# Kernel tuning notes

Hardware: AMD Instinct MI355X
Metric: run time of the kernel (lower is better)

## Reference

```python
import jax, jax.numpy as jnp
import numpy as np

TEMP = 0.1
NEG = -1e30  # stands in for removing the diagonal via masked_select
EPS = 1e-12  # F.normalize eps


def _l2norm(x, axis):
    n = jnp.linalg.norm(x, axis=axis, keepdims=True)
    return x / jnp.maximum(n, EPS)


def setup_inputs() -> dict:
    key = jax.random.key(0)
    k = jax.random.split(key, 6)
    B, D = 8192, 128      # instance batch, embed dim
    Bp, P = 256, 256      # patch batch, patches per sample
    v1_ins = jax.random.normal(k[0], (B, D), jnp.float32)
    v2_ins = jax.random.normal(k[1], (B, D), jnp.float32)
    v1_patch = jax.random.normal(k[2], (Bp, D, P), jnp.float32)
    v2_patch = jax.random.normal(k[3], (Bp, D, P), jnp.float32)
    v1_counts = jax.random.randint(k[4], (Bp, P), 0, 50, dtype=jnp.int32)
    v2_counts = jax.random.randint(k[5], (Bp, P), 0, 50, dtype=jnp.int32)
    return {"v1_ins": v1_ins, "v2_ins": v2_ins,
            "v1_patch": v1_patch, "v2_patch": v2_patch,
            "v1_counts": v1_counts, "v2_counts": v2_counts}


def _instance_ce(v1, v2):
    B = v1.shape[0]
    embs = jnp.concatenate([_l2norm(v1, 1), _l2norm(v2, 1)], axis=0)  # [2B, D]
    logits = (embs @ embs.T) / TEMP                                    # [2B, 2B]
    N = 2 * B
    # masking the diagonal to -inf == masked_select removal; positive of row i
    # is column (i+B) mod 2B (matches labels after diagonal removal shift)
    logits = jnp.where(jnp.eye(N, dtype=bool), NEG, logits)
    labels = jnp.concatenate([jnp.arange(B) + B, jnp.arange(B)])
    logp = jax.nn.log_softmax(logits, axis=1)
    return -jnp.mean(logp[jnp.arange(N), labels])


def _patch_ce(v1, v2, c1, c2):
    Bp, D, P = v1.shape
    embs = jnp.concatenate([_l2norm(v1, 1), _l2norm(v2, 1)], axis=2)   # [Bp, D, 2P]
    logits = jnp.einsum('bdi,bdj->bij', embs, embs) / TEMP             # [Bp, 2P, 2P]
    N = 2 * P
    logits = jnp.where(jnp.eye(N, dtype=bool)[None], NEG, logits)
    labels = jnp.concatenate([jnp.arange(P) + P, jnp.arange(P)])       # [2P]
    valid = ~jnp.concatenate([c1 == 0, c2 == 0], axis=1)               # [Bp, 2P]
    logp = jax.nn.log_softmax(logits, axis=2)
    pos = logp[:, jnp.arange(N), labels]                               # [Bp, 2P]
    # ignore_index=-100 -> mean over non-ignored elements
    n_valid = jnp.sum(valid.astype(logits.dtype))
    return -jnp.sum(jnp.where(valid, pos, 0.0)) / n_valid


def reference(v1_ins, v2_ins, v1_patch, v2_patch, v1_counts, v2_counts):
    ins_ce = _instance_ce(v1_ins, v2_ins)
    patch_ce = _patch_ce(v1_patch, v2_patch, v1_counts, v2_counts)
    return ins_ce + patch_ce
```

## Files before the change

### kernel.cpp

```cpp
#include <hip/hip_runtime.h>
#include <math.h>

typedef __bf16 bf16_t;
typedef __bf16 bf16x8 __attribute__((ext_vector_type(8)));
typedef float f32x4 __attribute__((ext_vector_type(4)));
typedef float f32x2 __attribute__((ext_vector_type(2)));

#define B_INS 8192
#define N_INS 16384
#define D 128
#define BP 256
#define P 256
#define NP 512

#define C1_CONST 14.426950408889634f

#define WS_ACC 0
#define WS_POS 8
#define WS_PPOS (WS_POS + N_INS)
#define NPAIRI 8128
#define WS_CI (WS_PPOS + BP * NP)
#define WS_RI (WS_CI + NPAIRI * 256)
#define WS_CP (WS_RI + 1088 * 256)
#define WS_RP (WS_CP + BP * 6 * 256)
#define WS_END (WS_RP + 1024 * 256)
#define EMB_I_BYTE ((((WS_END) * 4 + 15) / 16) * 16)
#define EMB_P_BYTE (EMB_I_BYTE + N_INS * D * 2)


#define NB_NORMI 128
#define NB_NORMP 2048
#define NB_PREP (NB_NORMI + NB_NORMP + 1)
#define NB_INS 1088
#define NB_PATCHB 1024
#define NB_GRAM (NB_INS + NB_PATCHB)
#define NB_FIN (128 + 256)

__device__ __forceinline__ void load_lds16(const bf16_t* g, bf16_t* l) {
    __builtin_amdgcn_global_load_lds(
        (const __attribute__((address_space(1))) void*)g,
        (__attribute__((address_space(3))) void*)l, 16, 0, 0);
}

__device__ __forceinline__ void stage_panel(const bf16_t* __restrict__ src,
                                            bf16_t* dst, int w, int lane) {
    const bf16_t* g = src + w * 4096 + lane * 8;
    bf16_t* d = dst + w * 4096;
#pragma unroll
    for (int it = 0; it < 8; it++)
        load_lds16(g + it * 512, d + it * 512);
}

__device__ __forceinline__ void load_afrags(const bf16_t* __restrict__ abase,
                                            int rh, int tx, int q, bf16x8 af[4][4]) {
    const bf16_t* a = abase + ((rh * 64 + tx) << 3);
#pragma unroll
    for (int rt = 0; rt < 4; rt++)
#pragma unroll
        for (int ks = 0; ks < 4; ks++)
            af[rt][ks] = *(const bf16x8*)(a + (((ks << 2) + q) << 10) + (rt << 7));
}

__global__ __launch_bounds__(256) void prep_k(const float* __restrict__ v1i,
                                              const float* __restrict__ v2i,
                                              const float* __restrict__ v1p,
                                              const float* __restrict__ v2p,
                                              bf16_t* __restrict__ embI,
                                              bf16_t* __restrict__ embP,
                                              float* __restrict__ ws) {
    __shared__ float L[128][65];
    __shared__ float ps[4][64];
    __shared__ float invs[128];
    int bx = blockIdx.x;
    int t = threadIdx.x;
    if (bx < NB_NORMI) {
        int p = bx;
        const float* srcP = (p < 64) ? (v1i + (size_t)p * 128 * D)
                                     : (v2i + (size_t)(p - 64) * 128 * D);
        {
            int r = t >> 1, h = t & 1;
            const float* row = srcP + (size_t)r * D + h * 64;
            float ss = 0.f;
#pragma unroll
            for (int j = 0; j < 16; j++) {
                float4 v = *(const float4*)(row + j * 4);
                ss += v.x * v.x + v.y * v.y + v.z * v.z + v.w * v.w;
            }
            ss += __shfl_xor(ss, 1, 64);
            if (h == 0) invs[r] = 1.0f / fmaxf(sqrtf(ss), 1e-12f);
        }
        __syncthreads();
#pragma unroll
        for (int it = 0; it < 8; it++) {
            int idx = it * 256 + t;
            int r = idx & 127, g = idx >> 7;
            const float* src8 = srcP + (size_t)r * D + g * 8;
            float4 a = *(const float4*)(src8);
            float4 b = *(const float4*)(src8 + 4);
            float inv = invs[r];
            bf16x8 v;
            v[0] = (bf16_t)(a.x * inv); v[1] = (bf16_t)(a.y * inv);
            v[2] = (bf16_t)(a.z * inv); v[3] = (bf16_t)(a.w * inv);
            v[4] = (bf16_t)(b.x * inv); v[5] = (bf16_t)(b.y * inv);
            v[6] = (bf16_t)(b.z * inv); v[7] = (bf16_t)(b.w * inv);
            *(bf16x8*)(embI + ((size_t)p << 14) + (g << 10) + (r << 3)) = v;
        }
    } else if (bx < NB_NORMI + NB_NORMP) {
        int bx2 = bx - NB_NORMI;
        int b = bx2 >> 3, h = (bx2 >> 2) & 1, chunk = bx2 & 3;
        int i0 = chunk * 64;
        const float* src = ((h == 0) ? v1p : v2p) + (size_t)b * D * P;
#pragma unroll
        for (int it = 0; it < 8; it++) {
            int fi = it * 256 + t;
            int d = fi >> 4, c4 = fi & 15;
            float4 v = *(const float4*)(src + (size_t)d * P + i0 + c4 * 4);
            L[d][c4 * 4 + 0] = v.x;
            L[d][c4 * 4 + 1] = v.y;
            L[d][c4 * 4 + 2] = v.z;
            L[d][c4 * 4 + 3] = v.w;
        }
        __syncthreads();
        {
            int col = t & 63, part = t >> 6;
            float ss = 0.f;
#pragma unroll 8
            for (int d = part * 32; d < part * 32 + 32; d++) { float x = L[d][col]; ss += x * x; }
            ps[part][col] = ss;
        }
        __syncthreads();
        if (t < 64) {
            float n2 = ps[0][t] + ps[1][t] + ps[2][t] + ps[3][t];
            invs[t] = 1.0f / fmaxf(sqrtf(n2), 1e-12f);
        }
        __syncthreads();
#pragma unroll
        for (int it = 0; it < 4; it++) {
            int idx = it * 256 + t;
            int ic = idx & 63, g = idx >> 6;
            float inv = invs[ic];
            bf16x8 v;
#pragma unroll
            for (int j = 0; j < 8; j++) v[j] = (bf16_t)(L[g * 8 + j][ic] * inv);
            int iLoc = h * P + i0 + ic;
            *(bf16x8*)(embP + ((size_t)b << 16) + ((size_t)(iLoc >> 7) << 14) +
                       (g << 10) + ((iLoc & 127) << 3)) = v;
        }
    } else {
        if (t < 8) ws[t] = 0.f;
    }
}

__global__ __launch_bounds__(256) void gram_k(const bf16_t* __restrict__ embI,
                                              const bf16_t* __restrict__ embP,
                                              float* __restrict__ pos,
                                              float* __restrict__ posp,
                                              float* __restrict__ colI,
                                              float* __restrict__ rowI,
                                              float* __restrict__ colP,
                                              float* __restrict__ rowP) {
    __shared__ __align__(16) bf16_t shB[2][16384];
    int t = threadIdx.x, w = t >> 6, lane = t & 63;
    int tx = lane & 15, q = lane >> 4;
    int rh = w & 1, ch = w >> 1;
    int bx = blockIdx.x;

    const bf16_t *Abase, *Bbase;
    float *posArr, *colArr, *rowDst;
    int R, c0, n, diagC, posC;
    if (bx < NB_INS) {
        int bid = bx, k = 0, cum = 0;
        while (bid >= cum + 8 * (16 - k)) { cum += 8 * (16 - k); k++; }
        int rem = bid - cum, cc = 16 - k;
        R = 8 * k + rem / cc;
        int ci = rem - (rem / cc) * cc;
        c0 = R + ci * 8;
        n = min(8, 128 - c0);
        Abase = embI + ((size_t)R << 14);
        Bbase = embI;
        posArr = pos;
        colArr = colI + (size_t)R * 256;
        rowDst = rowI + (size_t)(R * 16 + ci) * 256;
        diagC = R; posC = R + 64;
    } else {
        int pi = bx - NB_INS;
        int b = pi >> 2; R = pi & 3;
        c0 = R; n = 4 - R;
        const bf16_t* base = embP + ((size_t)b << 16);
        Abase = base + ((size_t)R << 14);
        Bbase = base;
        posArr = posp + (size_t)b * NP;
        colArr = colP + (size_t)(b * 6 + R) * 256;
        rowDst = rowP + (size_t)((b << 2) + R) * 256;
        diagC = R; posC = R + 2;
    }
    int rowBase = R * 128;

    bf16x8 af[4][4];
    load_afrags(Abase, rh, tx, q, af);

    f32x2 rowS2[8];
#pragma unroll
    for (int i = 0; i < 8; i++) rowS2[i] = (f32x2){0.f, 0.f};

    stage_panel(Bbase + ((size_t)c0 << 14), shB[0], w, lane);
    int cur = 0;
    for (int ti = 0; ti < n; ti++) {
        int C = c0 + ti;
        __syncthreads();
        if (ti + 1 < n)
            stage_panel(Bbase + ((size_t)(C + 1) << 14), shB[cur ^ 1], w, lane);
        bool isDiag = (C == diagC), isPos = (C == posC);
        int colBase = C * 128;
        const bf16_t* sb = shB[cur];

        float colS[4];
#pragma unroll
        for (int nt = 0; nt < 4; nt++) {
            bf16x8 bf[4];
#pragma unroll
            for (int ks = 0; ks < 4; ks++)
                bf[ks] = *(const bf16x8*)(sb + (((ks << 2) + q) << 10) +
                                          ((ch * 64 + nt * 16 + tx) << 3));
            f32x4 acc[4];
#pragma unroll
            for (int rt = 0; rt < 4; rt++) acc[rt] = (f32x4){0.f, 0.f, 0.f, 0.f};
#pragma unroll
            for (int ks = 0; ks < 4; ks++)
#pragma unroll
                for (int rt = 0; rt < 4; rt++)
                    acc[rt] = __builtin_amdgcn_mfma_f32_16x16x32_bf16(
                        af[rt][ks], bf[ks], acc[rt], 0, 0, 0);

            f32x2 cs = (f32x2){0.f, 0.f};
#pragma unroll
            for (int rt = 0; rt < 4; rt++) {
                f32x2 l0 = {acc[rt][0], acc[rt][1]};
                f32x2 l1 = {acc[rt][2], acc[rt][3]};
                l0 = l0 * C1_CONST - C1_CONST;
                l1 = l1 * C1_CONST - C1_CONST;
                f32x2 e0 = {__builtin_amdgcn_exp2f(l0.x), __builtin_amdgcn_exp2f(l0.y)};
                f32x2 e1 = {__builtin_amdgcn_exp2f(l1.x), __builtin_amdgcn_exp2f(l1.y)};
                if (isDiag) {
                    int inRow = rh * 64 + rt * 16 + q * 4;
                    int inCol = ch * 64 + nt * 16 + tx;
                    if (inRow + 0 == inCol) e0.x = 0.f;
                    if (inRow + 1 == inCol) e0.y = 0.f;
                    if (inRow + 2 == inCol) e1.x = 0.f;
                    if (inRow + 3 == inCol) e1.y = 0.f;
                }
                rowS2[rt * 2] += e0;
                rowS2[rt * 2 + 1] += e1;
                cs += e0 + e1;
            }
            colS[nt] = cs.x + cs.y;

            if (isPos && ch == rh) {
                int reg = tx - q * 4;
                if (reg >= 0 && reg < 4) {
                    float pl = acc[nt][reg] * 10.0f;
                    posArr[rowBase + rh * 64 + nt * 16 + tx] = pl;
                    posArr[colBase + rh * 64 + nt * 16 + tx] = pl;
                }
            }
        }
        if (!isDiag) {
#pragma unroll
            for (int i = 0; i < 4; i++) {
                colS[i] += __shfl_xor(colS[i], 16, 64);
                colS[i] += __shfl_xor(colS[i], 32, 64);
            }
            if (q == 0) {
                float* cdst = colArr + (size_t)(C * (C - 1) / 2) * 256 + rh * 128;
#pragma unroll
                for (int nt = 0; nt < 4; nt++)
                    cdst[ch * 64 + nt * 16 + tx] = colS[nt];
            }
        }
        cur ^= 1;
    }
    float* rowS = (float*)rowS2;
#pragma unroll
    for (int off = 1; off <= 8; off <<= 1)
#pragma unroll
        for (int i = 0; i < 16; i++) rowS[i] += __shfl_xor(rowS[i], off, 16);
    if (tx == 0) {
#pragma unroll
        for (int rt = 0; rt < 4; rt++)
#pragma unroll
            for (int reg = 0; reg < 4; reg++)
                rowDst[ch * 128 + rh * 64 + rt * 16 + q * 4 + reg] =
                    rowS[rt * 4 + reg];
    }
}

__global__ __launch_bounds__(256) void fin_k(const float* __restrict__ pos,
                                             const float* __restrict__ posp,
                                             const float* __restrict__ colI,
                                             const float* __restrict__ rowI,
                                             const float* __restrict__ colP,
                                             const float* __restrict__ rowP,
                                             const int* __restrict__ c1,
                                             const int* __restrict__ c2,
                                             float* __restrict__ acc,
                                             float* __restrict__ out) {
    int bx = blockIdx.x, t = threadIdx.x;
    int lane = t & 63, w = t >> 6;
    float va = 0.f, nv = 0.f;
    __shared__ float comb[128];
    if (bx < 128) {
        int p = bx;
        int half = t >> 7, r = t & 127;
        int cc = 16 - (p >> 3);
        float s = 0.f;
        const float* RIp = rowI + (size_t)(p * 16) * 256 + half * 128 + r;
        for (int ci = 0; ci < cc; ci++) s += RIp[ci * 256];
        const float* CIp = colI + (size_t)(p * (p - 1) / 2) * 256 + half * 128 + r;
        for (int Rq = 0; Rq < p; Rq++) s += CIp[Rq * 256];
        if (half == 1) comb[r] = s;
        __syncthreads();
        if (half == 0) {
            float S = s + comb[r];
            va = __logf(S) + 10.0f - pos[p * 128 + r];
        }
    } else {
        int b = bx - 128;
#pragma unroll
        for (int it = 0; it < 2; it++) {
            int idx = it * 256 + t;
            int p = idx >> 7, r = idx & 127;
            const float* RPp = rowP + (size_t)((b << 2) + p) * 256 + r;
            float s = RPp[0] + RPp[128];
            const float* CPp = colP + (size_t)(b * 6 + p * (p - 1) / 2) * 256 + r;
            for (int Rq = 0; Rq < p; Rq++) s += CPp[Rq * 256] + CPp[Rq * 256 + 128];
            int cnt = (idx < P) ? c1[b * P + idx] : c2[b * P + idx - P];
            if (cnt != 0) {
                va += __logf(s) + 10.0f - posp[b * NP + idx];
                nv += 1.0f;
            }
        }
    }
#pragma unroll
    for (int off = 32; off >= 1; off >>= 1) {
        va += __shfl_down(va, off, 64);
        nv += __shfl_down(nv, off, 64);
    }
    __shared__ float psum[4], pn[4];
    if (lane == 0) { psum[w] = va; pn[w] = nv; }
    __syncthreads();
    if (t == 0) {
        float sv = psum[0] + psum[1] + psum[2] + psum[3];
        float sn = pn[0] + pn[1] + pn[2] + pn[3];
        if (bx < 128) {
            atomicAdd(&acc[0], sv);
        } else {
            atomicAdd(&acc[1], sv);
            atomicAdd(&acc[2], sn);
        }
        __threadfence();
        unsigned old = atomicAdd((unsigned*)&acc[3], 1u);
        if (old == NB_FIN - 1) {
            float a0 = atomicAdd(&acc[0], 0.0f);
            float a1 = atomicAdd(&acc[1], 0.0f);
            float a2 = atomicAdd(&acc[2], 0.0f);
            out[0] = a0 * (1.0f / (float)N_INS) + a1 / a2;
        }
    }
}

extern "C" void kernel_launch(void* const* d_in, const int* in_sizes, int n_in,
                              void* d_out, int out_size, void* d_ws, size_t ws_size,
                              hipStream_t stream) {
    const float* v1i = (const float*)d_in[0];
    const float* v2i = (const float*)d_in[1];
    const float* v1p = (const float*)d_in[2];
    const float* v2p = (const float*)d_in[3];
    const int* c1 = (const int*)d_in[4];
    const int* c2 = (const int*)d_in[5];
    float* ws = (float*)d_ws;
    float* out = (float*)d_out;
    bf16_t* embI = (bf16_t*)((char*)d_ws + EMB_I_BYTE);
    bf16_t* embP = (bf16_t*)((char*)d_ws + EMB_P_BYTE);

    prep_k<<<NB_PREP, 256, 0, stream>>>(v1i, v2i, v1p, v2p, embI, embP, ws);
    gram_k<<<NB_GRAM, 256, 0, stream>>>(embI, embP, ws + WS_POS, ws + WS_PPOS,
                                        ws + WS_CI, ws + WS_RI,
                                        ws + WS_CP, ws + WS_RP);
    fin_k<<<NB_FIN, 256, 0, stream>>>(ws + WS_POS, ws + WS_PPOS, ws + WS_CI,
                                      ws + WS_RI, ws + WS_CP, ws + WS_RP,
                                      c1, c2, ws + WS_ACC, out);
}
```

Before: 226.5 us.

## Stage half panels in gram kernel to cut LDS and raise occupancy

The gram kernel now stages each 128-column B panel as two 64-column halves in a half-size LDS double buffer. The loop runs twice as many steps, each with half the MFMA work. Launch bounds now request 4 blocks per CU, and MFMA sections are wrapped in setprio so other waves can overlap. The fin kernel's strided reduction loops gain multiple accumulators and unrolling for more memory-level parallelism; the cost is more barriers and possible register pressure.

```diff
diff --git a/kernel.cpp b/kernel.cpp
--- a/kernel.cpp
+++ b/kernel.cpp
@@ -42,13 +42,13 @@
         (__attribute__((address_space(3))) void*)l, 16, 0, 0);
 }
 
-__device__ __forceinline__ void stage_panel(const bf16_t* __restrict__ src,
-                                            bf16_t* dst, int w, int lane) {
-    const bf16_t* g = src + w * 4096 + lane * 8;
-    bf16_t* d = dst + w * 4096;
-#pragma unroll
-    for (int it = 0; it < 8; it++)
-        load_lds16(g + it * 512, d + it * 512);
+__device__ __forceinline__ void stage_half(const bf16_t* __restrict__ srcHalf,
+                                           bf16_t* dst, int w, int lane) {
+#pragma unroll
+    for (int it = 0; it < 4; it++) {
+        int gp = w * 4 + it;
+        load_lds16(srcHalf + (gp << 10) + lane * 8, dst + (gp << 9));
+    }
 }
 
 __device__ __forceinline__ void load_afrags(const bf16_t* __restrict__ abase,
@@ -151,15 +151,15 @@
     }
 }
 
-__global__ __launch_bounds__(256) void gram_k(const bf16_t* __restrict__ embI,
-                                              const bf16_t* __restrict__ embP,
-                                              float* __restrict__ pos,
-                                              float* __restrict__ posp,
-                                              float* __restrict__ colI,
-                                              float* __restrict__ rowI,
-                                              float* __restrict__ colP,
-                                              float* __restrict__ rowP) {
-    __shared__ __align__(16) bf16_t shB[2][16384];
+__global__ __launch_bounds__(256, 4) void gram_k(const bf16_t* __restrict__ embI,
+                                                 const bf16_t* __restrict__ embP,
+                                                 float* __restrict__ pos,
+                                                 float* __restrict__ posp,
+                                                 float* __restrict__ colI,
+                                                 float* __restrict__ rowI,
+                                                 float* __restrict__ colP,
+                                                 float* __restrict__ rowP) {
+    __shared__ __align__(16) bf16_t shB[2][8192];
     int t = threadIdx.x, w = t >> 6, lane = t & 63;
     int tx = lane & 15, q = lane >> 4;
     int rh = w & 1, ch = w >> 1;
@@ -203,35 +203,41 @@
 #pragma unroll
     for (int i = 0; i < 8; i++) rowS2[i] = (f32x2){0.f, 0.f};
 
-    stage_panel(Bbase + ((size_t)c0 << 14), shB[0], w, lane);
+    int nSteps = n * 2;
+    stage_half(Bbase + ((size_t)c0 << 14), shB[0], w, lane);
     int cur = 0;
-    for (int ti = 0; ti < n; ti++) {
-        int C = c0 + ti;
-        __syncthreads();
-        if (ti + 1 < n)
-            stage_panel(Bbase + ((size_t)(C + 1) << 14), shB[cur ^ 1], w, lane);
+    for (int s = 0; s < nSteps; s++) {
+        int C = c0 + (s >> 1), h2 = s & 1;
+        __syncthreads();
+        if (s + 1 < nSteps) {
+            int C2 = c0 + ((s + 1) >> 1), h22 = (s + 1) & 1;
+            stage_half(Bbase + ((size_t)C2 << 14) + (h22 << 9), shB[cur ^ 1], w, lane);
+        }
         bool isDiag = (C == diagC), isPos = (C == posC);
         int colBase = C * 128;
         const bf16_t* sb = shB[cur];
 
-        float colS[4];
-#pragma unroll
-        for (int nt = 0; nt < 4; nt++) {
+        float colS[2];
+#pragma unroll
+        for (int nt = 0; nt < 2; nt++) {
+            int cp = ch * 32 + nt * 16 + tx;
             bf16x8 bf[4];
 #pragma unroll
             for (int ks = 0; ks < 4; ks++)
-                bf[ks] = *(const bf16x8*)(sb + (((ks << 2) + q) << 10) +
-                                          ((ch * 64 + nt * 16 + tx) << 3));
+                bf[ks] = *(const bf16x8*)(sb + (((ks << 2) + q) << 9) + (cp << 3));
             f32x4 acc[4];
 #pragma unroll
             for (int rt = 0; rt < 4; rt++) acc[rt] = (f32x4){0.f, 0.f, 0.f, 0.f};
+            __builtin_amdgcn_s_setprio(1);
 #pragma unroll
             for (int ks = 0; ks < 4; ks++)
 #pragma unroll
                 for (int rt = 0; rt < 4; rt++)
                     acc[rt] = __builtin_amdgcn_mfma_f32_16x16x32_bf16(
                         af[rt][ks], bf[ks], acc[rt], 0, 0, 0);
-
+            __builtin_amdgcn_s_setprio(0);
+
+            int inCol = h2 * 64 + cp;
             f32x2 cs = (f32x2){0.f, 0.f};
 #pragma unroll
             for (int rt = 0; rt < 4; rt++) {
@@ -243,7 +249,6 @@
                 f32x2 e1 = {__builtin_amdgcn_exp2f(l1.x), __builtin_amdgcn_exp2f(l1.y)};
                 if (isDiag) {
                     int inRow = rh * 64 + rt * 16 + q * 4;
-                    int inCol = ch * 64 + nt * 16 + tx;
                     if (inRow + 0 == inCol) e0.x = 0.f;
                     if (inRow + 1 == inCol) e0.y = 0.f;
                     if (inRow + 2 == inCol) e1.x = 0.f;
@@ -255,26 +260,28 @@
             }
             colS[nt] = cs.x + cs.y;
 
-            if (isPos && ch == rh) {
+            if (isPos && h2 == rh) {
                 int reg = tx - q * 4;
                 if (reg >= 0 && reg < 4) {
-                    float pl = acc[nt][reg] * 10.0f;
-                    posArr[rowBase + rh * 64 + nt * 16 + tx] = pl;
-                    posArr[colBase + rh * 64 + nt * 16 + tx] = pl;
+                    int rowOff = rh * 64 + (ch * 2 + nt) * 16 + tx;
+                    float pl = acc[ch * 2 + nt][reg] * 10.0f;
+                    posArr[rowBase + rowOff] = pl;
+                    posArr[colBase + rowOff] = pl;
                 }
             }
         }
         if (!isDiag) {
 #pragma unroll
-            for (int i = 0; i < 4; i++) {
+            for (int i = 0; i < 2; i++) {
                 colS[i] += __shfl_xor(colS[i], 16, 64);
                 colS[i] += __shfl_xor(colS[i], 32, 64);
             }
             if (q == 0) {
-                float* cdst = colArr + (size_t)(C * (C - 1) / 2) * 256 + rh * 128;
-#pragma unroll
-                for (int nt = 0; nt < 4; nt++)
-                    cdst[ch * 64 + nt * 16 + tx] = colS[nt];
+                float* cdst = colArr + (size_t)(C * (C - 1) / 2) * 256 + rh * 128 +
+                              h2 * 64;
+#pragma unroll
+                for (int nt = 0; nt < 2; nt++)
+                    cdst[ch * 32 + nt * 16 + tx] = colS[nt];
             }
         }
         cur ^= 1;
@@ -312,11 +319,22 @@
         int p = bx;
         int half = t >> 7, r = t & 127;
         int cc = 16 - (p >> 3);
-        float s = 0.f;
+        float s0 = 0.f, s1 = 0.f, s2 = 0.f, s3 = 0.f;
         const float* RIp = rowI + (size_t)(p * 16) * 256 + half * 128 + r;
-        for (int ci = 0; ci < cc; ci++) s += RIp[ci * 256];
+        int ci = 0;
+        for (; ci + 4 <= cc; ci += 4) {
+            s0 += RIp[ci * 256];       s1 += RIp[(ci + 1) * 256];
+            s2 += RIp[(ci + 2) * 256]; s3 += RIp[(ci + 3) * 256];
+        }
+        for (; ci < cc; ci++) s0 += RIp[ci * 256];
         const float* CIp = colI + (size_t)(p * (p - 1) / 2) * 256 + half * 128 + r;
-        for (int Rq = 0; Rq < p; Rq++) s += CIp[Rq * 256];
+        int Rq = 0;
+        for (; Rq + 4 <= p; Rq += 4) {
+            s0 += CIp[Rq * 256];       s1 += CIp[(Rq + 1) * 256];
+            s2 += CIp[(Rq + 2) * 256]; s3 += CIp[(Rq + 3) * 256];
+        }
+        for (; Rq < p; Rq++) s0 += CIp[Rq * 256];
+        float s = (s0 + s1) + (s2 + s3);
         if (half == 1) comb[r] = s;
         __syncthreads();
         if (half == 0) {
@@ -332,6 +350,7 @@
             const float* RPp = rowP + (size_t)((b << 2) + p) * 256 + r;
             float s = RPp[0] + RPp[128];
             const float* CPp = colP + (size_t)(b * 6 + p * (p - 1) / 2) * 256 + r;
+#pragma unroll 4
             for (int Rq = 0; Rq < p; Rq++) s += CPp[Rq * 256] + CPp[Rq * 256 + 128];
             int cnt = (idx < P) ? c1[b * P + idx] : c2[b * P + idx - P];
             if (cnt != 0) {
```

New measurement: 392.4 us. 73.2% more time.

## Replace async LDS double buffer with register-staged prefetch and swizzle block order

Applied to the files above, without the earlier changes.

The gram kernel stops using global_load_lds into two LDS buffers. It now prefetches the next B panel into registers while the current panel is computed, then writes it into a single LDS buffer between two barriers. This halves shared memory per block, which may let more blocks reside per CU, at the cost of extra VGPRs and an additional barrier per tile. Block indices are also remapped to interleave work across groups of eight, which is meant to balance load and locality across CUs.

```diff
diff --git a/kernel.cpp b/kernel.cpp
--- a/kernel.cpp
+++ b/kernel.cpp
@@ -35,21 +35,6 @@
 #define NB_PATCHB 1024
 #define NB_GRAM (NB_INS + NB_PATCHB)
 #define NB_FIN (128 + 256)
-
-__device__ __forceinline__ void load_lds16(const bf16_t* g, bf16_t* l) {
-    __builtin_amdgcn_global_load_lds(
-        (const __attribute__((address_space(1))) void*)g,
-        (__attribute__((address_space(3))) void*)l, 16, 0, 0);
-}
-
-__device__ __forceinline__ void stage_panel(const bf16_t* __restrict__ src,
-                                            bf16_t* dst, int w, int lane) {
-    const bf16_t* g = src + w * 4096 + lane * 8;
-    bf16_t* d = dst + w * 4096;
-#pragma unroll
-    for (int it = 0; it < 8; it++)
-        load_lds16(g + it * 512, d + it * 512);
-}
 
 __device__ __forceinline__ void load_afrags(const bf16_t* __restrict__ abase,
                                             int rh, int tx, int q, bf16x8 af[4][4]) {
@@ -159,11 +144,12 @@
                                               float* __restrict__ rowI,
                                               float* __restrict__ colP,
                                               float* __restrict__ rowP) {
-    __shared__ __align__(16) bf16_t shB[2][16384];
+    __shared__ __align__(16) bf16_t shB[16384];
     int t = threadIdx.x, w = t >> 6, lane = t & 63;
     int tx = lane & 15, q = lane >> 4;
     int rh = w & 1, ch = w >> 1;
-    int bx = blockIdx.x;
+    int bx0 = blockIdx.x;
+    int bx = (bx0 & 7) * (NB_GRAM / 8) + (bx0 >> 3);
 
     const bf16_t *Abase, *Bbase;
     float *posArr, *colArr, *rowDst;
@@ -203,16 +189,31 @@
 #pragma unroll
     for (int i = 0; i < 8; i++) rowS2[i] = (f32x2){0.f, 0.f};
 
-    stage_panel(Bbase + ((size_t)c0 << 14), shB[0], w, lane);
-    int cur = 0;
+    bf16x8 rg[8];
+    {
+        const bf16_t* srcP = Bbase + ((size_t)c0 << 14);
+#pragma unroll
+        for (int it = 0; it < 8; it++)
+            rg[it] = *(const bf16x8*)(srcP + ((it * 256 + t) << 3));
+#pragma unroll
+        for (int it = 0; it < 8; it++)
+            *(bf16x8*)(shB + ((it * 256 + t) << 3)) = rg[it];
+    }
+    __syncthreads();
+
     for (int ti = 0; ti < n; ti++) {
         int C = c0 + ti;
-        __syncthreads();
-        if (ti + 1 < n)
-            stage_panel(Bbase + ((size_t)(C + 1) << 14), shB[cur ^ 1], w, lane);
+        if (ti + 1 < n) {
+            const bf16_t* srcN = Bbase + ((size_t)(C + 1) << 14);
+#pragma unroll
+            for (int it = 0; it < 8; it++)
+                rg[it] = *(const bf16x8*)(srcN + ((it * 256 + t) << 3));
+        }
+        __builtin_amdgcn_sched_barrier(0);
+
         bool isDiag = (C == diagC), isPos = (C == posC);
         int colBase = C * 128;
-        const bf16_t* sb = shB[cur];
+        const bf16_t* sb = shB;
 
         float colS[4];
 #pragma unroll
@@ -277,7 +278,13 @@
                     cdst[ch * 64 + nt * 16 + tx] = colS[nt];
             }
         }
-        cur ^= 1;
+        if (ti + 1 < n) {
+            __syncthreads();
+#pragma unroll
+            for (int it = 0; it < 8; it++)
+                *(bf16x8*)(shB + ((it * 256 + t) << 3)) = rg[it];
+            __syncthreads();
+        }
     }
     float* rowS = (float*)rowS2;
 #pragma unroll
```

Result: slower. 313.8 us (+38.6%).

## Split gram tiles into column halves to double blocks and halve LDS

Applied to the files above, without the earlier changes.

Each gram block now handles only one 64-column half of each 128-column B panel. This doubles the grid and halves the shared-memory panel buffers, and launch bounds request 4 blocks per SM for higher occupancy. Row partial sums are written per half, so the finalize kernel reads twice as many row partials. In exchange, each block reloads the same A fragments, duplicating A-fragment global traffic, and the row-sum workspace grows.

```diff
diff --git a/kernel.cpp b/kernel.cpp
--- a/kernel.cpp
+++ b/kernel.cpp
@@ -21,9 +21,9 @@
 #define NPAIRI 8128
 #define WS_CI (WS_PPOS + BP * NP)
 #define WS_RI (WS_CI + NPAIRI * 256)
-#define WS_CP (WS_RI + 1088 * 256)
+#define WS_CP (WS_RI + 2176 * 256)
 #define WS_RP (WS_CP + BP * 6 * 256)
-#define WS_END (WS_RP + 1024 * 256)
+#define WS_END (WS_RP + 2048 * 256)
 #define EMB_I_BYTE ((((WS_END) * 4 + 15) / 16) * 16)
 #define EMB_P_BYTE (EMB_I_BYTE + N_INS * D * 2)
 
@@ -31,8 +31,8 @@
 #define NB_NORMI 128
 #define NB_NORMP 2048
 #define NB_PREP (NB_NORMI + NB_NORMP + 1)
-#define NB_INS 1088
-#define NB_PATCHB 1024
+#define NB_INS 2176
+#define NB_PATCHB 2048
 #define NB_GRAM (NB_INS + NB_PATCHB)
 #define NB_FIN (128 + 256)
 
@@ -42,13 +42,14 @@
         (__attribute__((address_space(3))) void*)l, 16, 0, 0);
 }
 
-__device__ __forceinline__ void stage_panel(const bf16_t* __restrict__ src,
-                                            bf16_t* dst, int w, int lane) {
-    const bf16_t* g = src + w * 4096 + lane * 8;
-    bf16_t* d = dst + w * 4096;
-#pragma unroll
-    for (int it = 0; it < 8; it++)
-        load_lds16(g + it * 512, d + it * 512);
+__device__ __forceinline__ void stage_half(const bf16_t* __restrict__ src,
+                                           bf16_t* dst, int w, int lane, int cb) {
+    const bf16_t* g = src + (cb << 9) + lane * 8;
+#pragma unroll
+    for (int it = 0; it < 4; it++) {
+        int gp = w * 4 + it;
+        load_lds16(g + (gp << 10), dst + (gp << 9));
+    }
 }
 
 __device__ __forceinline__ void load_afrags(const bf16_t* __restrict__ abase,
@@ -151,47 +152,49 @@
     }
 }
 
-__global__ __launch_bounds__(256) void gram_k(const bf16_t* __restrict__ embI,
-                                              const bf16_t* __restrict__ embP,
-                                              float* __restrict__ pos,
-                                              float* __restrict__ posp,
-                                              float* __restrict__ colI,
-                                              float* __restrict__ rowI,
-                                              float* __restrict__ colP,
-                                              float* __restrict__ rowP) {
-    __shared__ __align__(16) bf16_t shB[2][16384];
+__global__ __launch_bounds__(256, 4) void gram_k(const bf16_t* __restrict__ embI,
+                                                 const bf16_t* __restrict__ embP,
+                                                 float* __restrict__ pos,
+                                                 float* __restrict__ posp,
+                                                 float* __restrict__ colI,
+                                                 float* __restrict__ rowI,
+                                                 float* __restrict__ colP,
+                                                 float* __restrict__ rowP) {
+    __shared__ __align__(16) bf16_t shB[2][8192];
     int t = threadIdx.x, w = t >> 6, lane = t & 63;
     int tx = lane & 15, q = lane >> 4;
-    int rh = w & 1, ch = w >> 1;
+    int rh = w & 1, sub = w >> 1;
     int bx = blockIdx.x;
 
     const bf16_t *Abase, *Bbase;
     float *posArr, *colArr, *rowDst;
-    int R, c0, n, diagC, posC;
+    int R, c0, n, diagC, posC, cb;
     if (bx < NB_INS) {
-        int bid = bx, k = 0, cum = 0;
+        int inner = bx >> 1; cb = bx & 1;
+        int bid = inner, k = 0, cum = 0;
         while (bid >= cum + 8 * (16 - k)) { cum += 8 * (16 - k); k++; }
-        int rem = bid - cum, cc = 16 - k;
-        R = 8 * k + rem / cc;
-        int ci = rem - (rem / cc) * cc;
+        int rem = bid - cum, cc2 = 16 - k;
+        R = 8 * k + rem / cc2;
+        int ci = rem - (rem / cc2) * cc2;
         c0 = R + ci * 8;
         n = min(8, 128 - c0);
         Abase = embI + ((size_t)R << 14);
         Bbase = embI;
         posArr = pos;
         colArr = colI + (size_t)R * 256;
-        rowDst = rowI + (size_t)(R * 16 + ci) * 256;
+        rowDst = rowI + (size_t)((R * 16 + ci) * 2 + cb) * 256;
         diagC = R; posC = R + 64;
     } else {
         int pi = bx - NB_INS;
-        int b = pi >> 2; R = pi & 3;
+        int inner = pi >> 1; cb = pi & 1;
+        int b = inner >> 2; R = inner & 3;
         c0 = R; n = 4 - R;
         const bf16_t* base = embP + ((size_t)b << 16);
         Abase = base + ((size_t)R << 14);
         Bbase = base;
         posArr = posp + (size_t)b * NP;
         colArr = colP + (size_t)(b * 6 + R) * 256;
-        rowDst = rowP + (size_t)((b << 2) + R) * 256;
+        rowDst = rowP + (size_t)((((b << 2) + R) * 2) + cb) * 256;
         diagC = R; posC = R + 2;
     }
     int rowBase = R * 128;
@@ -203,25 +206,25 @@
 #pragma unroll
     for (int i = 0; i < 8; i++) rowS2[i] = (f32x2){0.f, 0.f};
 
-    stage_panel(Bbase + ((size_t)c0 << 14), shB[0], w, lane);
+    stage_half(Bbase + ((size_t)c0 << 14), shB[0], w, lane, cb);
     int cur = 0;
     for (int ti = 0; ti < n; ti++) {
         int C = c0 + ti;
         __syncthreads();
         if (ti + 1 < n)
-            stage_panel(Bbase + ((size_t)(C + 1) << 14), shB[cur ^ 1], w, lane);
+            stage_half(Bbase + ((size_t)(C + 1) << 14), shB[cur ^ 1], w, lane, cb);
         bool isDiag = (C == diagC), isPos = (C == posC);
         int colBase = C * 128;
         const bf16_t* sb = shB[cur];
 
-        float colS[4];
-#pragma unroll
-        for (int nt = 0; nt < 4; nt++) {
+        float colS[2];
+#pragma unroll
+        for (int nt = 0; nt < 2; nt++) {
+            int cl = sub * 32 + nt * 16 + tx;
             bf16x8 bf[4];
 #pragma unroll
             for (int ks = 0; ks < 4; ks++)
-                bf[ks] = *(const bf16x8*)(sb + (((ks << 2) + q) << 10) +
-                                          ((ch * 64 + nt * 16 + tx) << 3));
+                bf[ks] = *(const bf16x8*)(sb + (((ks << 2) + q) << 9) + (cl << 3));
             f32x4 acc[4];
 #pragma unroll
             for (int rt = 0; rt < 4; rt++) acc[rt] = (f32x4){0.f, 0.f, 0.f, 0.f};
@@ -232,6 +235,7 @@
                     acc[rt] = __builtin_amdgcn_mfma_f32_16x16x32_bf16(
                         af[rt][ks], bf[ks], acc[rt], 0, 0, 0);
 
+            int inCol = cb * 64 + cl;
             f32x2 cs = (f32x2){0.f, 0.f};
 #pragma unroll
             for (int rt = 0; rt < 4; rt++) {
@@ -243,7 +247,6 @@
                 f32x2 e1 = {__builtin_amdgcn_exp2f(l1.x), __builtin_amdgcn_exp2f(l1.y)};
                 if (isDiag) {
                     int inRow = rh * 64 + rt * 16 + q * 4;
-                    int inCol = ch * 64 + nt * 16 + tx;
                     if (inRow + 0 == inCol) e0.x = 0.f;
                     if (inRow + 1 == inCol) e0.y = 0.f;
                     if (inRow + 2 == inCol) e1.x = 0.f;
@@ -255,26 +258,28 @@
             }
             colS[nt] = cs.x + cs.y;
 
-            if (isPos && ch == rh) {
+            if (isPos && cb == rh) {
                 int reg = tx - q * 4;
                 if (reg >= 0 && reg < 4) {
-                    float pl = acc[nt][reg] * 10.0f;
-                    posArr[rowBase + rh * 64 + nt * 16 + tx] = pl;
-                    posArr[colBase + rh * 64 + nt * 16 + tx] = pl;
+                    f32x4 av = sub ? acc[2 + nt] : acc[nt];
+                    int rowOff = rh * 64 + (sub * 2 + nt) * 16 + tx;
+                    float pl = av[reg] * 10.0f;
+                    posArr[rowBase + rowOff] = pl;
+                    posArr[colBase + rowOff] = pl;
                 }
             }
         }
         if (!isDiag) {
 #pragma unroll
-            for (int i = 0; i < 4; i++) {
+            for (int i = 0; i < 2; i++) {
                 colS[i] += __shfl_xor(colS[i], 16, 64);
                 colS[i] += __shfl_xor(colS[i], 32, 64);
             }
             if (q == 0) {
                 float* cdst = colArr + (size_t)(C * (C - 1) / 2) * 256 + rh * 128;
 #pragma unroll
-                for (int nt = 0; nt < 4; nt++)
-                    cdst[ch * 64 + nt * 16 + tx] = colS[nt];
+                for (int nt = 0; nt < 2; nt++)
+                    cdst[cb * 64 + sub * 32 + nt * 16 + tx] = colS[nt];
             }
         }
         cur ^= 1;
@@ -289,7 +294,7 @@
         for (int rt = 0; rt < 4; rt++)
 #pragma unroll
             for (int reg = 0; reg < 4; reg++)
-                rowDst[ch * 128 + rh * 64 + rt * 16 + q * 4 + reg] =
+                rowDst[sub * 128 + rh * 64 + rt * 16 + q * 4 + reg] =
                     rowS[rt * 4 + reg];
     }
 }
@@ -313,8 +318,8 @@
         int half = t >> 7, r = t & 127;
         int cc = 16 - (p >> 3);
         float s = 0.f;
-        const float* RIp = rowI + (size_t)(p * 16) * 256 + half * 128 + r;
-        for (int ci = 0; ci < cc; ci++) s += RIp[ci * 256];
+        const float* RIp = rowI + (size_t)p * 8192 + half * 128 + r;
+        for (int ci = 0; ci < cc; ci++) s += RIp[ci * 512] + RIp[ci * 512 + 256];
         const float* CIp = colI + (size_t)(p * (p - 1) / 2) * 256 + half * 128 + r;
         for (int Rq = 0; Rq < p; Rq++) s += CIp[Rq * 256];
         if (half == 1) comb[r] = s;
@@ -329,8 +334,8 @@
         for (int it = 0; it < 2; it++) {
             int idx = it * 256 + t;
             int p = idx >> 7, r = idx & 127;
-            const float* RPp = rowP + (size_t)((b << 2) + p) * 256 + r;
-            float s = RPp[0] + RPp[128];
+            const float* RPp = rowP + (size_t)((b << 2) + p) * 512 + r;
+            float s = RPp[0] + RPp[128] + RPp[256] + RPp[384];
             const float* CPp = colP + (size_t)(b * 6 + p * (p - 1) / 2) * 256 + r;
             for (int Rq = 0; Rq < p; Rq++) s += CPp[Rq * 256] + CPp[Rq * 256 + 128];
             int cnt = (idx < P) ? c1[b * P + idx] : c2[b * P + idx - P];
```

Result: slower. 324.3 us (+43.2%).
